# Performance work log

Hardware: AMD Instinct MI355X
Metric: run time of the kernel (lower is better)

## Reference

```python
import jax, jax.numpy as jnp
import numpy as np

V = 50000      # node_num
E = 200000     # number of edges
LN = 128       # feat_dim
S = 32         # stat_dim
C = 10         # num_class
T = 2          # propagation steps
MU = 0.9


def setup_inputs() -> dict:
    key = jax.random.key(0)
    ks = jax.random.split(key, 10)
    feat_Matrix = jax.random.normal(ks[0], (V, LN), dtype=jnp.float32)
    X_Node = jax.random.randint(ks[1], (E,), 0, V, dtype=jnp.int32)
    X_Neis = jax.random.randint(ks[2], (E,), 0, V, dtype=jnp.int32)
    # degrees >= 1 (divided by in Hw)
    dg_list = jax.random.randint(ks[3], (E,), 1, 33).astype(jnp.float32)
    sc = 0.02
    Wxi = jax.random.normal(ks[4], (2 * LN, S * S), dtype=jnp.float32) * sc
    bxi = jnp.zeros((S * S,), dtype=jnp.float32)
    Wrou = jax.random.normal(ks[5], (LN, S), dtype=jnp.float32) * sc
    brou = jnp.zeros((S,), dtype=jnp.float32)
    Wout = jax.random.normal(ks[6], (S, C), dtype=jnp.float32) * sc
    bout = jnp.zeros((C,), dtype=jnp.float32)
    return {
        "feat_Matrix": feat_Matrix, "X_Node": X_Node, "X_Neis": X_Neis,
        "dg_list": dg_list, "Wxi": Wxi, "bxi": bxi,
        "Wrou": Wrou, "brou": brou, "Wout": Wout, "bout": bout,
    }


def reference(feat_Matrix, X_Node, X_Neis, dg_list,
              Wxi, bxi, Wrou, brou, Wout, bout):
    # Gather endpoint features: X = [feat[u] || feat[v]]  -> [E, 2*LN]
    X = jnp.concatenate(
        (feat_Matrix[X_Node], feat_Matrix[X_Neis]), axis=1)

    # Xi(X): per-edge transition matrix A  [E, S, S], scaled by mu/s/deg
    A = jnp.tanh(X @ Wxi + bxi).reshape(E, S, S)
    A = A * (MU / S) / dg_list[:, None, None]
    # Rou on first chunk (= node features)  [E, S]
    b = jnp.tanh(X[:, :LN] @ Wrou + brou)

    H = jnp.zeros((V, S), dtype=feat_Matrix.dtype)
    for _ in range(T):
        He = H[X_Node]                                  # gather  [E, S]
        He = jnp.einsum('eij,ej->ei', A, He) + b        # per-edge transition
        # scatter-add per node (equivalent to AggrSum's dense mask matmul)
        H = jax.ops.segment_sum(He, X_Node, num_segments=V)

    # dropout is identity at inference
    return jax.nn.log_softmax(H @ Wout + bout, axis=-1)
```

## Files before the change

### kernel.cpp

```cpp
#include <hip/hip_runtime.h>

#define EE 200000
#define VV 50000
#define LN 128
#define KD 256
#define SS 32
#define NN 1024
#define CC 10
#define MUS 0.028125f

typedef short short8_t __attribute__((ext_vector_type(8)));
typedef float f32x4 __attribute__((ext_vector_type(4)));

__device__ __forceinline__ unsigned short f32_to_bf16_rne(float f) {
    union { float f; unsigned u; } x; x.f = f;
    unsigned r = x.u + 0x7FFFu + ((x.u >> 16) & 1u);
    return (unsigned short)(r >> 16);
}

__device__ __forceinline__ float bf16_to_f32(unsigned short h) {
    union { unsigned u; float f; } x; x.u = ((unsigned)h) << 16; return x.f;
}

__device__ __forceinline__ float tanh_fast(float x) {
    float t = __builtin_amdgcn_exp2f(x * 2.885390081777927f);
    return 1.0f - 2.0f * __builtin_amdgcn_rcpf(t + 1.0f);
}

__device__ __forceinline__ float ptanh(float x) {
    float x2 = x * x;
    return x * (27.f + x2) * __builtin_amdgcn_rcpf(27.f + 9.f * x2);
}

__device__ __forceinline__ void load_lds16(const void* g, void* l) {
    __builtin_amdgcn_global_load_lds(
        (const __attribute__((address_space(1))) unsigned int*)g,
        (__attribute__((address_space(3))) unsigned int*)l,
        16, 0, 0);
}

__global__ void k_prep(const float* __restrict__ feat, unsigned short* __restrict__ featB,
                       const float* __restrict__ Wxi, unsigned short* __restrict__ WxiB,
                       const float* __restrict__ bxi, float* __restrict__ bxiT,
                       const int* __restrict__ Xn, int* __restrict__ cnt,
                       const float* __restrict__ Wrou, const float* __restrict__ brou,
                       float* __restrict__ R) {
    int b = blockIdx.x, tid = threadIdx.x;
    if (b < 6250) {
        int idx = b * 256 + tid;
        float4 v = ((const float4*)feat)[idx];
        ushort4 o;
        o.x = f32_to_bf16_rne(v.x); o.y = f32_to_bf16_rne(v.y);
        o.z = f32_to_bf16_rne(v.z); o.w = f32_to_bf16_rne(v.w);
        ((ushort4*)featB)[idx] = o;
    } else if (b < 7274) {
        int idx = (b - 6250) * 256 + tid;
        int k = idx >> 10, ncol = idx & 1023;
        int np = ((ncol & 31) << 5) | (ncol >> 5);
        WxiB[((size_t)(k >> 3) * NN + np) * 8 + (k & 7)] = f32_to_bf16_rne(Wxi[idx]);
    } else if (b == 7274) {
        #pragma unroll
        for (int it = 0; it < 4; ++it) {
            int i = it * 256 + tid;
            bxiT[i] = bxi[(i & 31) * 32 + (i >> 5)];
        }
    } else if (b < 8057) {
        int e = (b - 7275) * 256 + tid;
        if (e < EE) atomicAdd(&cnt[Xn[e]], 1);
    } else {
        int gid = (b - 8057) * 256 + tid;
        int u = gid >> 5, s = gid & 31;
        const float* fr = feat + (size_t)u * LN;
        float a = brou[s];
        #pragma unroll 8
        for (int k = 0; k < LN; ++k) a += fr[k] * Wrou[k * SS + s];
        R[gid] = tanh_fast(a);
    }
}

__global__ void __launch_bounds__(256) k_scan_lb(const int* __restrict__ cnt,
                                                 int* __restrict__ rowptr,
                                                 int* __restrict__ cursor,
                                                 unsigned int* flags) {
    __shared__ int s[256];
    __shared__ int bp;
    int b = blockIdx.x, tid = threadIdx.x;
    int i = b * 256 + tid;
    int x = (i < VV) ? cnt[i] : 0;
    s[tid] = x; __syncthreads();
    int v = x;
    #pragma unroll
    for (int off = 1; off < 256; off <<= 1) {
        int t = (tid >= off) ? s[tid - off] : 0;
        __syncthreads();
        v += t; s[tid] = v;
        __syncthreads();
    }
    int agg = s[255];

    if (b == 0) {
        if (tid == 0) {
            bp = 0;
            atomicExch(&flags[0], 0x80000000u | (unsigned)agg);
        }
    } else {
        if (tid == 0)
            atomicExch(&flags[b], 0x40000000u | (unsigned)agg);
        if (tid < 64) {
            int lane = tid;
            int base = b - 1;
            int pref = 0;
            while (true) {
                int idx = base - lane;
                unsigned wv;
                if (idx >= 0) {
                    do { wv = atomicAdd(&flags[idx], 0u); } while ((wv & 0xC0000000u) == 0u);
                } else {
                    wv = 0x80000000u;
                }
                bool isP = (wv >= 0x80000000u);
                unsigned long long bal = __ballot(isP);
                int Lp = bal ? __builtin_ctzll(bal) : 64;
                int val = (int)(wv & 0x3FFFFFFFu);
                int contrib = (lane < Lp) ? val : ((lane == Lp && bal) ? val : 0);
                #pragma unroll
                for (int o = 1; o < 64; o <<= 1) contrib += __shfl_xor(contrib, o);
                pref += contrib;
                if (bal) break;
                base -= 64;
            }
            if (lane == 0) {
                bp = pref;
                atomicExch(&flags[b], 0x80000000u | (unsigned)(pref + agg));
            }
        }
    }
    __syncthreads();
    int excl = v - x + bp;
    if (i < VV) { rowptr[i] = excl; cursor[i] = excl; }
    if (b == 0 && tid == 0) rowptr[VV] = EE;
}

__global__ void k_scatter(const int* __restrict__ Xn, int* __restrict__ cursor,
                          int* __restrict__ perm) {
    int e = blockIdx.x * 256 + threadIdx.x;
    if (e < EE) {
        int p = atomicAdd(&cursor[Xn[e]], 1);
        perm[p] = e;
    }
}

__global__ void __launch_bounds__(256, 3)
k_edge_gemm(const unsigned short* __restrict__ featB, const unsigned short* __restrict__ WxiB,
            const int* __restrict__ Xn, const int* __restrict__ Xe,
            const float* __restrict__ dg, const float* __restrict__ bxiT,
            const int* __restrict__ perm, const float* __restrict__ R,
            const int* __restrict__ rowptr, unsigned short* __restrict__ HeB) {
    __shared__ __align__(16) unsigned short Bs[2 * 8192];
    __shared__ float hs[128][33];
    __shared__ int   us[128], vs[128];
    __shared__ float scale_s[128];

    const int tid = threadIdx.x;
    const int eb = blockIdx.x * 128;

    const size_t qbase = (size_t)((tid >> 5) * 16384 + (tid & 31) * 16);
    const int    dbase = tid * 16;

#define STAGE_CH(cc, slot) { \
    const char* gs_ = (const char*)WxiB + (size_t)((cc) * 512) + qbase; \
    char* ld_ = (char*)Bs + (slot) * 16384 + dbase; \
    load_lds16(gs_,          ld_); \
    load_lds16(gs_ + 131072, ld_ + 4096); \
    load_lds16(gs_ + 262144, ld_ + 8192); \
    load_lds16(gs_ + 393216, ld_ + 12288); }

    STAGE_CH(0, 0);

    if (tid < 128) {
        int p = eb + tid; if (p > EE - 1) p = EE - 1;
        int e0 = perm[p];
        int u = Xn[e0];
        us[tid] = u; vs[tid] = Xe[e0];
        scale_s[tid] = MUS / dg[e0];
    }
    __syncthreads();

    const int w = tid >> 6, lane = tid & 63;
    const int g = lane >> 4, l15 = lane & 15;
    const int row0 = w * 32;

    short8_t af[8][2];
    #pragma unroll
    for (int kk = 0; kk < 8; ++kk)
        #pragma unroll
        for (int mf = 0; mf < 2; ++mf) {
            int el = row0 + mf * 16 + l15;
            int node = (kk < 4) ? us[el] : vs[el];
            af[kk][mf] = *(const short8_t*)(featB + (size_t)node * LN + (kk & 3) * 32 + g * 8);
        }

    #pragma unroll
    for (int it = 0; it < 16; ++it) {
        int idx = it * 256 + tid;
        int el = idx >> 5, s2 = idx & 31;
        int u = us[el];
        float cnt = (float)(rowptr[u + 1] - rowptr[u]);
        hs[el][s2] = cnt * R[u * SS + s2];
    }
    __syncthreads();

    const char* bbase = (const char*)Bs + (g * 512 + l15 * 16);
    const f32x4 z4 = {0.f, 0.f, 0.f, 0.f};
    f32x4 accA[2][2], accB[2][2], he[2][2];
    #pragma unroll
    for (int mf = 0; mf < 2; ++mf)
        #pragma unroll
        for (int f = 0; f < 2; ++f) he[mf][f] = z4;

#define MFMA_CH(slot, cur) { \
    const char* bs_ = bbase + (slot) * 16384; \
    _Pragma("unroll") \
    for (int kk = 0; kk < 8; ++kk) { \
        short8_t b0 = *(const short8_t*)(bs_ + kk * 2048); \
        short8_t b1 = *(const short8_t*)(bs_ + kk * 2048 + 256); \
        _Pragma("unroll") \
        for (int mf = 0; mf < 2; ++mf) { \
            cur[mf][0] = __builtin_amdgcn_mfma_f32_16x16x32_bf16(af[kk][mf], b0, kk ? cur[mf][0] : z4, 0, 0, 0); \
            cur[mf][1] = __builtin_amdgcn_mfma_f32_16x16x32_bf16(af[kk][mf], b1, kk ? cur[mf][1] : z4, 0, 0, 0); } } }

#define EPI_CH(j, prev) { \
    float bx0 = bxiT[(j) * 32 + l15]; \
    float bx1 = bxiT[(j) * 32 + 16 + l15]; \
    _Pragma("unroll") \
    for (int mf = 0; mf < 2; ++mf) \
        _Pragma("unroll") \
        for (int r = 0; r < 4; ++r) { \
            float hv = hs[row0 + mf * 16 + g * 4 + r][j]; \
            he[mf][0][r] += ptanh(prev[mf][0][r] + bx0) * hv; \
            he[mf][1][r] += ptanh(prev[mf][1][r] + bx1) * hv; } }

#define SYNCPT() { \
    asm volatile("s_waitcnt vmcnt(0)" ::: "memory"); \
    __builtin_amdgcn_s_barrier(); \
    __builtin_amdgcn_sched_barrier(0); }

    #pragma unroll 1
    for (int c = 0; c < 32; c += 2) {
        STAGE_CH(c + 1, 1);
        MFMA_CH(0, accA);
        if (c) EPI_CH(c - 1, accB);
        SYNCPT();

        if (c + 2 < 32) STAGE_CH(c + 2, 0);
        MFMA_CH(1, accB);
        EPI_CH(c, accA);
        SYNCPT();
    }
    EPI_CH(31, accB);

    #pragma unroll
    for (int mf = 0; mf < 2; ++mf)
        #pragma unroll
        for (int r = 0; r < 4; ++r) {
            int el = row0 + mf * 16 + g * 4 + r;
            int ep = eb + el;
            if (ep < EE) {
                float sc = scale_s[el];
                HeB[(size_t)ep * SS + l15]      = f32_to_bf16_rne(he[mf][0][r] * sc);
                HeB[(size_t)ep * SS + 16 + l15] = f32_to_bf16_rne(he[mf][1][r] * sc);
            }
        }
#undef STAGE_CH
#undef MFMA_CH
#undef EPI_CH
#undef SYNCPT
}

__global__ void k_reduce_out(const unsigned short* __restrict__ HeB, const int* __restrict__ rowptr,
                             const float* __restrict__ R, const float* __restrict__ Wout,
                             const float* __restrict__ bout, float* __restrict__ out) {
    __shared__ float h2[8][33];
    __shared__ float lgS[8][10];
    __shared__ float lseS[8];
    int tid = threadIdx.x;
    int un8 = tid >> 5, s = tid & 31;
    int u = blockIdx.x * 8 + un8;
    int p0 = rowptr[u], p1 = rowptr[u + 1];
    float acc = (float)(p1 - p0) * R[u * SS + s];
    for (int p = p0; p < p1; ++p)
        acc += bf16_to_f32(HeB[(size_t)p * SS + s]);
    h2[un8][s] = acc;
    __syncthreads();
    if (tid < 80) {
        int un = tid / 10, c = tid - un * 10;
        float a = bout[c];
        #pragma unroll
        for (int s2 = 0; s2 < SS; ++s2) a += h2[un][s2] * Wout[s2 * CC + c];
        lgS[un][c] = a;
    }
    __syncthreads();
    if (tid < 8) {
        float mx = lgS[tid][0];
        #pragma unroll
        for (int c = 1; c < CC; ++c) mx = fmaxf(mx, lgS[tid][c]);
        float se = 0.f;
        #pragma unroll
        for (int c = 0; c < CC; ++c)
            se += __builtin_amdgcn_exp2f((lgS[tid][c] - mx) * 1.4426950408889634f);
        lseS[tid] = mx + __builtin_amdgcn_logf(se) * 0.6931471805599453f;
    }
    __syncthreads();
    if (tid < 80) {
        int un = tid / 10, c = tid - un * 10;
        out[(size_t)(blockIdx.x * 8 + un) * CC + c] = lgS[un][c] - lseS[un];
    }
}

extern "C" void kernel_launch(void* const* d_in, const int* in_sizes, int n_in,
                              void* d_out, int out_size, void* d_ws, size_t ws_size,
                              hipStream_t stream) {
    const float* feat = (const float*)d_in[0];
    const int*   Xn   = (const int*)d_in[1];
    const int*   Xe   = (const int*)d_in[2];
    const float* dg   = (const float*)d_in[3];
    const float* Wxi  = (const float*)d_in[4];
    const float* bxi  = (const float*)d_in[5];
    const float* Wrou = (const float*)d_in[6];
    const float* brou = (const float*)d_in[7];
    const float* Wout = (const float*)d_in[8];
    const float* bout = (const float*)d_in[9];
    float* out = (float*)d_out;

    char* ws = (char*)d_ws;
    unsigned short* featB  = (unsigned short*)(ws);
    unsigned short* WxiB   = (unsigned short*)(ws + 12800000);
    unsigned short* HeB    = (unsigned short*)(ws + 13324288);
    float*          R      = (float*)(ws + 26124288);
    int*            perm   = (int*)(ws + 32524288);
    int*            rowptr = (int*)(ws + 33324288);
    int*            cursor = (int*)(ws + 33524352);
    int*            cnt    = (int*)(ws + 33724352);
    unsigned int*   flags  = (unsigned int*)(ws + 33924352);
    float*          bxiT   = (float*)(ws + 33925376);

    hipMemsetAsync(cnt, 0, 201024, stream);

    k_prep      <<<14307, 256, 0, stream>>>(feat, featB, Wxi, WxiB, bxi, bxiT, Xn, cnt,
                                            Wrou, brou, R);
    k_scan_lb   <<<196, 256, 0, stream>>>(cnt, rowptr, cursor, flags);
    k_scatter   <<<782, 256, 0, stream>>>(Xn, cursor, perm);
    k_edge_gemm <<<(EE + 127) / 128, 256, 0, stream>>>(featB, WxiB, Xn, Xe, dg, bxiT, perm, R, rowptr, HeB);
    k_reduce_out<<<VV / 8, 256, 0, stream>>>(HeB, rowptr, R, Wout, bout, out);
}
```

Measured before the change: 303.9 us.

## Halve Wxi LDS staging and drop ping-pong accumulators to raise occupancy

Splits each 256-K chunk of Wxi into two half-K stages of 8 KB each, which halves the LDS double buffer. The two alternating accumulator sets are replaced by a single one, and the tanh epilogue now runs right after each chunk's MFMAs. Launch bounds go from 3 to 4 blocks per CU, aiming for more waves in flight to hide gather and LDS latency. In exchange, barriers per chunk double and the epilogue no longer overlaps the next chunk's MFMAs.

New measurement: 304.0 us. Within noise of the previous version (+0.1%).

```diff
diff --git a/kernel.cpp b/kernel.cpp
--- a/kernel.cpp
+++ b/kernel.cpp
@@ -150,13 +150,13 @@
     }
 }
 
-__global__ void __launch_bounds__(256, 3)
+__global__ void __launch_bounds__(256, 4)
 k_edge_gemm(const unsigned short* __restrict__ featB, const unsigned short* __restrict__ WxiB,
             const int* __restrict__ Xn, const int* __restrict__ Xe,
             const float* __restrict__ dg, const float* __restrict__ bxiT,
             const int* __restrict__ perm, const float* __restrict__ R,
             const int* __restrict__ rowptr, unsigned short* __restrict__ HeB) {
-    __shared__ __align__(16) unsigned short Bs[2 * 8192];
+    __shared__ __align__(16) unsigned short Bs[2 * 4096];
     __shared__ float hs[128][33];
     __shared__ int   us[128], vs[128];
     __shared__ float scale_s[128];
@@ -164,24 +164,21 @@
     const int tid = threadIdx.x;
     const int eb = blockIdx.x * 128;
 
-    const size_t qbase = (size_t)((tid >> 5) * 16384 + (tid & 31) * 16);
-    const int    dbase = tid * 16;
-
-#define STAGE_CH(cc, slot) { \
-    const char* gs_ = (const char*)WxiB + (size_t)((cc) * 512) + qbase; \
-    char* ld_ = (char*)Bs + (slot) * 16384 + dbase; \
+    const size_t gq0 = (size_t)((tid >> 5) * 16384 + (tid & 31) * 16);
+    const int d0 = tid * 16;
+
+#define STAGE_H(cc, hh, slot) { \
+    const char* gs_ = (const char*)WxiB + (size_t)(hh) * 262144 + (size_t)(cc) * 512 + gq0; \
+    char* ld_ = (char*)Bs + (slot) * 8192 + d0; \
     load_lds16(gs_,          ld_); \
-    load_lds16(gs_ + 131072, ld_ + 4096); \
-    load_lds16(gs_ + 262144, ld_ + 8192); \
-    load_lds16(gs_ + 393216, ld_ + 12288); }
-
-    STAGE_CH(0, 0);
+    load_lds16(gs_ + 131072, ld_ + 4096); }
+
+    STAGE_H(0, 0, 0);
 
     if (tid < 128) {
         int p = eb + tid; if (p > EE - 1) p = EE - 1;
         int e0 = perm[p];
-        int u = Xn[e0];
-        us[tid] = u; vs[tid] = Xe[e0];
+        us[tid] = Xn[e0]; vs[tid] = Xe[e0];
         scale_s[tid] = MUS / dg[e0];
     }
     __syncthreads();
@@ -212,33 +209,11 @@
 
     const char* bbase = (const char*)Bs + (g * 512 + l15 * 16);
     const f32x4 z4 = {0.f, 0.f, 0.f, 0.f};
-    f32x4 accA[2][2], accB[2][2], he[2][2];
+    f32x4 acc[2][2], he[2][2];
     #pragma unroll
     for (int mf = 0; mf < 2; ++mf)
         #pragma unroll
         for (int f = 0; f < 2; ++f) he[mf][f] = z4;
-
-#define MFMA_CH(slot, cur) { \
-    const char* bs_ = bbase + (slot) * 16384; \
-    _Pragma("unroll") \
-    for (int kk = 0; kk < 8; ++kk) { \
-        short8_t b0 = *(const short8_t*)(bs_ + kk * 2048); \
-        short8_t b1 = *(const short8_t*)(bs_ + kk * 2048 + 256); \
-        _Pragma("unroll") \
-        for (int mf = 0; mf < 2; ++mf) { \
-            cur[mf][0] = __builtin_amdgcn_mfma_f32_16x16x32_bf16(af[kk][mf], b0, kk ? cur[mf][0] : z4, 0, 0, 0); \
-            cur[mf][1] = __builtin_amdgcn_mfma_f32_16x16x32_bf16(af[kk][mf], b1, kk ? cur[mf][1] : z4, 0, 0, 0); } } }
-
-#define EPI_CH(j, prev) { \
-    float bx0 = bxiT[(j) * 32 + l15]; \
-    float bx1 = bxiT[(j) * 32 + 16 + l15]; \
-    _Pragma("unroll") \
-    for (int mf = 0; mf < 2; ++mf) \
-        _Pragma("unroll") \
-        for (int r = 0; r < 4; ++r) { \
-            float hv = hs[row0 + mf * 16 + g * 4 + r][j]; \
-            he[mf][0][r] += ptanh(prev[mf][0][r] + bx0) * hv; \
-            he[mf][1][r] += ptanh(prev[mf][1][r] + bx1) * hv; } }
 
 #define SYNCPT() { \
     asm volatile("s_waitcnt vmcnt(0)" ::: "memory"); \
@@ -246,18 +221,45 @@
     __builtin_amdgcn_sched_barrier(0); }
 
     #pragma unroll 1
-    for (int c = 0; c < 32; c += 2) {
-        STAGE_CH(c + 1, 1);
-        MFMA_CH(0, accA);
-        if (c) EPI_CH(c - 1, accB);
+    for (int c = 0; c < 32; ++c) {
+        STAGE_H(c, 1, 1);
+        #pragma unroll
+        for (int kk = 0; kk < 4; ++kk) {
+            short8_t b0 = *(const short8_t*)(bbase + kk * 2048);
+            short8_t b1 = *(const short8_t*)(bbase + kk * 2048 + 256);
+            #pragma unroll
+            for (int mf = 0; mf < 2; ++mf) {
+                acc[mf][0] = __builtin_amdgcn_mfma_f32_16x16x32_bf16(af[kk][mf], b0, kk ? acc[mf][0] : z4, 0, 0, 0);
+                acc[mf][1] = __builtin_amdgcn_mfma_f32_16x16x32_bf16(af[kk][mf], b1, kk ? acc[mf][1] : z4, 0, 0, 0);
+            }
+        }
         SYNCPT();
 
-        if (c + 2 < 32) STAGE_CH(c + 2, 0);
-        MFMA_CH(1, accB);
-        EPI_CH(c, accA);
+        if (c < 31) STAGE_H(c + 1, 0, 0);
+        #pragma unroll
+        for (int kk = 4; kk < 8; ++kk) {
+            short8_t b0 = *(const short8_t*)(bbase + 8192 + (kk - 4) * 2048);
+            short8_t b1 = *(const short8_t*)(bbase + 8192 + (kk - 4) * 2048 + 256);
+            #pragma unroll
+            for (int mf = 0; mf < 2; ++mf) {
+                acc[mf][0] = __builtin_amdgcn_mfma_f32_16x16x32_bf16(af[kk][mf], b0, acc[mf][0], 0, 0, 0);
+                acc[mf][1] = __builtin_amdgcn_mfma_f32_16x16x32_bf16(af[kk][mf], b1, acc[mf][1], 0, 0, 0);
+            }
+        }
+        {
+            float bx0 = bxiT[c * 32 + l15];
+            float bx1 = bxiT[c * 32 + 16 + l15];
+            #pragma unroll
+            for (int mf = 0; mf < 2; ++mf)
+                #pragma unroll
+                for (int r = 0; r < 4; ++r) {
+                    float hv = hs[row0 + mf * 16 + g * 4 + r][c];
+                    he[mf][0][r] += ptanh(acc[mf][0][r] + bx0) * hv;
+                    he[mf][1][r] += ptanh(acc[mf][1][r] + bx1) * hv;
+                }
+        }
         SYNCPT();
     }
-    EPI_CH(31, accB);
 
     #pragma unroll
     for (int mf = 0; mf < 2; ++mf)
@@ -271,9 +273,7 @@
                 HeB[(size_t)ep * SS + 16 + l15] = f32_to_bf16_rne(he[mf][1][r] * sc);
             }
         }
-#undef STAGE_CH
-#undef MFMA_CH
-#undef EPI_CH
+#undef STAGE_H
 #undef SYNCPT
 }
 
```
